# Optimization experiments

Hardware: AMD Instinct MI355X
Metric: run time of the kernel (lower is better)

Reference implementation:

```python
import jax, jax.numpy as jnp
import numpy as np
import math

B, T = 4, 2048
V = 512          # vocab_size
D = 256          # d_model
H = 4            # n_heads
NLAYERS = 2
DH = D // H      # d_head = 64
NB = DH // 2     # n_blocks = 32
R = 2            # bottleneck_r
DFF = 4 * D
GRID = 64
EPS = 1e-5


def setup_inputs() -> dict:
    key = jax.random.key(0)
    ks = iter(jax.random.split(key, 32))
    def nrm(shape, s=0.02):
        return jax.random.normal(next(ks), shape, dtype=jnp.float32) * s
    tokens = jax.random.randint(next(ks), (B, T), 0, V)
    token_emb = nrm((V, D))
    # low-rank action-to-Lie projection
    w_in = nrm((D, R))
    w_out = nrm((R, H * NB))
    # geometric omega init (PathIntegrator.__init__)
    frac = jnp.arange(NB, dtype=jnp.float32) / max(NB - 1, 1)
    omega = jnp.broadcast_to(2.0 * math.pi * (1.0 / GRID) ** frac, (H, NB)).astype(jnp.float32)
    # stacked per-layer params (weights stored [in, out])
    Wq = nrm((NLAYERS, D, D)); bq = jnp.zeros((NLAYERS, D), jnp.float32)
    Wk = nrm((NLAYERS, D, D)); bk = jnp.zeros((NLAYERS, D), jnp.float32)
    Wv = nrm((NLAYERS, D, D)); bv = jnp.zeros((NLAYERS, D), jnp.float32)
    Wo = nrm((NLAYERS, D, D)); bo = jnp.zeros((NLAYERS, D), jnp.float32)
    ln1_g = jnp.ones((NLAYERS, D), jnp.float32); ln1_b = jnp.zeros((NLAYERS, D), jnp.float32)
    ln2_g = jnp.ones((NLAYERS, D), jnp.float32); ln2_b = jnp.zeros((NLAYERS, D), jnp.float32)
    W1 = nrm((NLAYERS, D, DFF)); b1 = jnp.zeros((NLAYERS, DFF), jnp.float32)
    W2 = nrm((NLAYERS, DFF, D)); b2 = jnp.zeros((NLAYERS, D), jnp.float32)
    out_g = jnp.ones((D,), jnp.float32); out_b = jnp.zeros((D,), jnp.float32)
    Wout = nrm((D, V)); bout = jnp.zeros((V,), jnp.float32)
    return dict(tokens=tokens, token_emb=token_emb, w_in=w_in, w_out=w_out, omega=omega,
                Wq=Wq, bq=bq, Wk=Wk, bk=bk, Wv=Wv, bv=bv, Wo=Wo, bo=bo,
                ln1_g=ln1_g, ln1_b=ln1_b, ln2_g=ln2_g, ln2_b=ln2_b,
                W1=W1, b1=b1, W2=W2, b2=b2, out_g=out_g, out_b=out_b,
                Wout=Wout, bout=bout)


def _ln(x, g, b):
    mu = jnp.mean(x, axis=-1, keepdims=True)
    xc = x - mu
    var = jnp.mean(xc * xc, axis=-1, keepdims=True)
    return xc * jax.lax.rsqrt(var + EPS) * g + b


def _rope(x, cos, sin):
    # x: (B,H,T,DH); cos/sin: (B,H,T,NB) with NB = DH//2 (interleaved pairs)
    x1 = x[..., 0::2]
    x2 = x[..., 1::2]
    o1 = x1 * cos - x2 * sin
    o2 = x1 * sin + x2 * cos
    return jnp.stack([o1, o2], axis=-1).reshape(x.shape)


def reference(tokens, token_emb, w_in, w_out, omega, Wq, bq, Wk, bk, Wv, bv, Wo, bo,
              ln1_g, ln1_b, ln2_g, ln2_b, W1, b1, W2, b2, out_g, out_b, Wout, bout):
    Bx, Tx = tokens.shape
    x = token_emb[tokens]                                   # (B,T,D)
    # action -> Lie algebra deltas (low rank)
    delta = ((x @ w_in) @ w_out).reshape(Bx, Tx, H, NB)     # (B,T,H,NB)
    # path integrator: cumulative angles
    angles = jnp.cumsum(delta, axis=1) * omega[None, None]  # (B,T,H,NB)
    angles = angles.transpose(0, 2, 1, 3)                   # (B,H,T,NB)
    cos_a, sin_a = jnp.cos(angles), jnp.sin(angles)
    causal = jnp.triu(jnp.ones((Tx, Tx), bool), 1)          # True = masked
    neg = jnp.finfo(x.dtype).min
    scale = 1.0 / math.sqrt(DH)
    for i in range(NLAYERS):
        h = _ln(x, ln1_g[i], ln1_b[i])
        Q = (h @ Wq[i] + bq[i]).reshape(Bx, Tx, H, DH).transpose(0, 2, 1, 3)
        K = (h @ Wk[i] + bk[i]).reshape(Bx, Tx, H, DH).transpose(0, 2, 1, 3)
        Vv = (h @ Wv[i] + bv[i]).reshape(Bx, Tx, H, DH).transpose(0, 2, 1, 3)
        Q = _rope(Q, cos_a, sin_a)
        K = _rope(K, cos_a, sin_a)
        scores = jnp.einsum('bhqd,bhkd->bhqk', Q, K) * scale
        scores = jnp.where(causal, neg, scores)
        attn = jax.nn.softmax(scores, axis=-1)
        out = jnp.einsum('bhqk,bhkd->bhqd', attn, Vv)
        out = out.transpose(0, 2, 1, 3).reshape(Bx, Tx, D)
        x = x + out @ Wo[i] + bo[i]
        h2 = _ln(x, ln2_g[i], ln2_b[i])
        x = x + jax.nn.gelu(h2 @ W1[i] + b1[i], approximate=False) @ W2[i] + b2[i]
    x = _ln(x, out_g, out_b)
    return x @ Wout + bout                                   # (B,T,V)
```

## Files before the change

### kernel.cpp

```cpp
#include <hip/hip_runtime.h>
#include <hip/hip_bf16.h>
#include <math.h>

#define B_   4
#define T_   2048
#define V_   512
#define D_   256
#define H_   4
#define DH_  64
#define NB_  32
#define DFF_ 1024
#define NL_  2

typedef __attribute__((ext_vector_type(8))) short short8_t;
typedef __attribute__((ext_vector_type(4))) float float4_t;

#define MFMA16(a,b,c) __builtin_amdgcn_mfma_f32_16x16x32_bf16(a,b,c,0,0,0)

__device__ __forceinline__ unsigned short f2bf_bits(float f) {
    unsigned u = __float_as_uint(f);
    u += 0x7fffu + ((u >> 16) & 1u);
    return (unsigned short)(u >> 16);
}

__global__ __launch_bounds__(256) void wt_kernel(
    const float* __restrict__ Wq, const float* __restrict__ Wk,
    const float* __restrict__ Wv, const float* __restrict__ Wo,
    const float* __restrict__ W1, const float* __restrict__ W2,
    const float* __restrict__ Wout,
    unsigned short* __restrict__ wqt, unsigned short* __restrict__ wkt,
    unsigned short* __restrict__ wvt, unsigned short* __restrict__ wot,
    unsigned short* __restrict__ w1t, unsigned short* __restrict__ w2t,
    unsigned short* __restrict__ woutt)
{
    __shared__ float tile[32][33];
    int bx = blockIdx.x, tid = threadIdx.x;
    const float* src; unsigned short* dst; int Kd, Nd, tr, tc;
    if (bx < 512) {
        int am = bx >> 6, t = bx & 63;
        const float* s4[4] = {Wq, Wk, Wv, Wo};
        unsigned short* d4[4] = {wqt, wkt, wvt, wot};
        src = s4[am >> 1] + (long)(am & 1) * 65536;
        dst = d4[am >> 1] + (long)(am & 1) * 65536;
        Kd = 256; Nd = 256; tr = t >> 3; tc = t & 7;
    } else if (bx < 1024) {
        int idx = bx - 512, mat = idx >> 8, t = idx & 255;
        src = W1 + (long)mat * 262144; dst = w1t + (long)mat * 262144;
        Kd = 256; Nd = 1024; tr = t >> 5; tc = t & 31;
    } else if (bx < 1536) {
        int idx = bx - 1024, mat = idx >> 8, t = idx & 255;
        src = W2 + (long)mat * 262144; dst = w2t + (long)mat * 262144;
        Kd = 1024; Nd = 256; tr = t >> 3; tc = t & 7;
    } else {
        int t = bx - 1536;
        src = Wout; dst = woutt; Kd = 256; Nd = 512; tr = t >> 4; tc = t & 15;
    }
    int kr = tid >> 3, nc4 = (tid & 7) * 4;
    float4_t v = *(const float4_t*)&src[(long)(tr * 32 + kr) * Nd + tc * 32 + nc4];
    for (int j = 0; j < 4; ++j) tile[kr][nc4 + j] = v[j];
    __syncthreads();
    int nr = tid >> 3, kc4 = (tid & 7) * 4;
    unsigned short tmp[4];
    for (int j = 0; j < 4; ++j) tmp[j] = f2bf_bits(tile[kc4 + j][nr]);
    uint2 uu;
    uu.x = (unsigned)tmp[0] | ((unsigned)tmp[1] << 16);
    uu.y = (unsigned)tmp[2] | ((unsigned)tmp[3] << 16);
    *(uint2*)&dst[(long)(tc * 32 + nr) * Kd + tr * 32 + kc4] = uu;
}

__global__ __launch_bounds__(256) void embed_kernel(
    const int* __restrict__ tokens, const float* __restrict__ emb,
    const float* __restrict__ w_in, const float* __restrict__ w_out,
    float* __restrict__ x, float* __restrict__ delta)
{
    int bt = blockIdx.x;
    int d  = threadIdx.x;
    int tok = tokens[bt];
    float e = emb[tok * D_ + d];
    x[(long)bt * D_ + d] = e;

    __shared__ float r0s[256], r1s[256];
    r0s[d] = e * w_in[d * 2 + 0];
    r1s[d] = e * w_in[d * 2 + 1];
    __syncthreads();
    for (int off = 128; off > 0; off >>= 1) {
        if (d < off) { r0s[d] += r0s[d + off]; r1s[d] += r1s[d + off]; }
        __syncthreads();
    }
    float r0 = r0s[0], r1 = r1s[0];
    if (d < H_ * NB_) {
        delta[(long)bt * (H_ * NB_) + d] =
            r0 * w_out[d] + r1 * w_out[H_ * NB_ + d];
    }
}

__global__ __launch_bounds__(256) void cumsum_kernel(
    const float* __restrict__ delta, const float* __restrict__ omega,
    float* __restrict__ cosb, float* __restrict__ sinb)
{
    int c = blockIdx.x & (H_ * NB_ - 1);
    int b = blockIdx.x >> 7;
    int tid = threadIdx.x;
    float om = omega[c];
    int h = c >> 5, nb = c & (NB_ - 1);

    float vals[8];
    float s = 0.0f;
    for (int i = 0; i < 8; ++i) {
        int t = tid * 8 + i;
        vals[i] = delta[((long)b * T_ + t) * (H_ * NB_) + c];
        s += vals[i];
    }
    __shared__ float sc[256];
    sc[tid] = s;
    __syncthreads();
    for (int off = 1; off < 256; off <<= 1) {
        float v = (tid >= off) ? sc[tid - off] : 0.0f;
        __syncthreads();
        sc[tid] += v;
        __syncthreads();
    }
    float run = sc[tid] - s;
    for (int i = 0; i < 8; ++i) {
        run += vals[i];
        float ang = run * om;
        int t = tid * 8 + i;
        long oi = ((long)(b * H_ + h) * T_ + t) * NB_ + nb;
        cosb[oi] = cosf(ang);
        sinb[oi] = sinf(ang);
    }
}

__global__ __launch_bounds__(256) void ln_kernel(
    const float* __restrict__ x, const float* __restrict__ g,
    const float* __restrict__ b, unsigned short* __restrict__ out)
{
    int w = threadIdx.x >> 6, lane = threadIdx.x & 63;
    long row = (long)blockIdx.x * 4 + w;
    float4_t v = *(const float4_t*)&x[row * D_ + lane * 4];
    float s = v[0] + v[1] + v[2] + v[3];
    float q = v[0]*v[0] + v[1]*v[1] + v[2]*v[2] + v[3]*v[3];
    for (int off = 1; off < 64; off <<= 1) {
        s += __shfl_xor(s, off);
        q += __shfl_xor(q, off);
    }
    float mu  = s * (1.0f / D_);
    float var = q * (1.0f / D_) - mu * mu;
    float inv = rsqrtf(var + 1e-5f);
    float4_t gg = *(const float4_t*)&g[lane * 4];
    float4_t bb = *(const float4_t*)&b[lane * 4];
    unsigned short h0 = f2bf_bits((v[0] - mu) * inv * gg[0] + bb[0]);
    unsigned short h1 = f2bf_bits((v[1] - mu) * inv * gg[1] + bb[1]);
    unsigned short h2 = f2bf_bits((v[2] - mu) * inv * gg[2] + bb[2]);
    unsigned short h3 = f2bf_bits((v[3] - mu) * inv * gg[3] + bb[3]);
    uint2 uu;
    uu.x = (unsigned)h0 | ((unsigned)h1 << 16);
    uu.y = (unsigned)h2 | ((unsigned)h3 << 16);
    *(uint2*)&out[row * D_ + lane * 4] = uu;
}

__global__ __launch_bounds__(256) void gemm_mfma(
    const unsigned short* __restrict__ A, const unsigned short* __restrict__ Bt,
    const float* __restrict__ bias, const float* __restrict__ res,
    float* __restrict__ outf, unsigned short* __restrict__ outb,
    const float* __restrict__ ropeC, const float* __restrict__ ropeS,
    float qscale, int M, int N, int K, int mode, int do_gelu)
{
    __shared__ __align__(16) short As[64 * 72];
    __shared__ __align__(16) short Bs[64 * 72];
    int tid = threadIdx.x;
    int w = tid >> 6, lane = tid & 63, quad = lane >> 4, l16 = lane & 15;
    int n0 = blockIdx.x * 64, r0 = blockIdx.y * 64;

    float4_t acc[4];
    for (int nt = 0; nt < 4; ++nt) acc[nt] = (float4_t){0.f, 0.f, 0.f, 0.f};

    for (int k0 = 0; k0 < K; k0 += 64) {
        __syncthreads();
        for (int i = 0; i < 2; ++i) {
            int e = tid + 256 * i;
            int r = e >> 3, c8 = e & 7;
            *(short8_t*)&As[r * 72 + c8 * 8] =
                *(const short8_t*)&A[(long)(r0 + r) * K + k0 + c8 * 8];
            *(short8_t*)&Bs[r * 72 + c8 * 8] =
                *(const short8_t*)&Bt[(long)(n0 + r) * K + k0 + c8 * 8];
        }
        __syncthreads();
        for (int kq = 0; kq < 2; ++kq) {
            short8_t a = *(const short8_t*)&As[(w * 16 + l16) * 72 + kq * 32 + quad * 8];
            for (int nt = 0; nt < 4; ++nt) {
                short8_t bfr = *(const short8_t*)&Bs[(nt * 16 + l16) * 72 + kq * 32 + quad * 8];
                acc[nt] = MFMA16(a, bfr, acc[nt]);
            }
        }
    }

    int h_head = n0 >> 6;
    for (int nt = 0; nt < 4; ++nt) {
        int n = n0 + nt * 16 + l16;
        float bcol = (mode == 2) ? 0.0f : bias[n];
        for (int r = 0; r < 4; ++r) {
            int row = r0 + w * 16 + quad * 4 + r;
            float v = acc[nt][r] + ((mode == 2) ? bias[row] : bcol);
            if (res) v += res[(long)row * N + n];
            if (do_gelu) v = 0.5f * v * (1.0f + erff(v * 0.70710678118654752f));
            if (mode == 0) {
                outf[(long)row * N + n] = v;
            } else if (mode == 1 || mode == 2) {
                outb[(long)row * N + n] = f2bf_bits(v);
            } else {
                float vp = __shfl_xor(v, 1);
                int bb = row >> 11, t = row & (T_ - 1);
                int nb = (n & 63) >> 1;
                long ci = ((long)(bb * H_ + h_head) * T_ + t) * NB_ + nb;
                float c = ropeC[ci], sn = ropeS[ci];
                float ov = (l16 & 1) ? (vp * sn + v * c) : (v * c - vp * sn);
                outb[((long)(bb * H_ + h_head) * T_ + t) * DH_ + (n & 63)] =
                    f2bf_bits(ov * qscale);
            }
        }
    }
}

__global__ __launch_bounds__(512) void attn_mfma(
    const unsigned short* __restrict__ Qb, const unsigned short* __restrict__ Kb,
    const unsigned short* __restrict__ Vt, unsigned short* __restrict__ O)
{
    __shared__ __align__(16) short KsS[2][64 * 72];
    __shared__ __align__(16) short VsS[2][64 * 72];
    union PsOm { short Ps[8][16 * 72]; float Om[4][16 * 66]; };
    __shared__ __align__(16) PsOm U;
    __shared__ float Ml[4][16][2];

    int tid = threadIdx.x;
    int w = tid >> 6, lane = tid & 63;
    int quad = lane >> 4, l16 = lane & 15;
    int bh = blockIdx.x & 15;
    int p  = blockIdx.x >> 4;
    int wr = w & 3;
    int g  = w >> 2;
    int b = bh >> 2, h = bh & 3;
    int qtS = 31 - p;

    const unsigned short* kgb = Kb + (long)bh * T_ * DH_;
    const unsigned short* vgb = Vt + (long)h * DH_ * (B_ * T_) + (long)b * T_;
    short* PsW = &U.Ps[w][0];

    int row0 = wr * 16 + (lane >> 3);
    int c80  = (lane & 7) * 8;

    int q0 = (g == 0 ? p : qtS) * 64;
    int qglob = q0 + wr * 16 + l16;
    const unsigned short* qp =
        Qb + ((long)bh * T_ + q0 + wr * 16 + l16) * DH_ + quad * 8;
    short8_t aq[2];
    aq[0] = *(const short8_t*)qp;
    aq[1] = *(const short8_t*)(qp + 32);

    float m_r = -3.0e38f, l_r = 0.0f;
    float4_t o[4];
    for (int nt = 0; nt < 4; ++nt) o[nt] = (float4_t){0.f, 0.f, 0.f, 0.f};

    {
        int k0n = (g == 0) ? 0 : (16 - p) * 64;
        for (int i = 0; i < 2; ++i) {
            int row = row0 + 8 * i;
            short8_t kv = *(const short8_t*)&kgb[(long)(k0n + row) * DH_ + c80];
            short8_t vv = *(const short8_t*)&vgb[(long)row * (B_ * T_) + k0n + c80];
            *(short8_t*)&KsS[g][row * 72 + c80] = kv;
            *(short8_t*)&VsS[g][row * 72 + c80] = vv;
        }
    }
    __syncthreads();

    for (int j = 0; j < 17; ++j) {
        bool idle  = (g == 1) && (j == 16);
        bool haveN = (j < 16) && !((g == 1) && (j == 15));

        short8_t stK[2], stV[2];
        if (haveN) {
            int jn = j + 1;
            int k0n = (g == 0) ? ((jn <= p) ? jn * 64 : (jn - p - 1) * 64)
                               : (16 - p + jn) * 64;
            for (int i = 0; i < 2; ++i) {
                int row = row0 + 8 * i;
                stK[i] = *(const short8_t*)&kgb[(long)(k0n + row) * DH_ + c80];
                stV[i] = *(const short8_t*)&vgb[(long)row * (B_ * T_) + k0n + c80];
            }
        }

        if (!idle) {
            int k0 = (g == 0) ? ((j <= p) ? j * 64 : (j - p - 1) * 64)
                              : (16 - p + j) * 64;
            bool msk = (g == 0) ? (j == p) : (j == 15);

            short8_t kf[4][2], vb[4][2];
            for (int nt = 0; nt < 4; ++nt) {
                const short* kb_ = &KsS[g][(nt * 16 + l16) * 72 + quad * 8];
                const short* vb_ = &VsS[g][(nt * 16 + l16) * 72 + quad * 8];
                kf[nt][0] = *(const short8_t*)kb_;
                kf[nt][1] = *(const short8_t*)(kb_ + 32);
                vb[nt][0] = *(const short8_t*)vb_;
                vb[nt][1] = *(const short8_t*)(vb_ + 32);
            }

            float4_t st[4];
            for (int nt = 0; nt < 4; ++nt) {
                float4_t sa = (float4_t){0.f, 0.f, 0.f, 0.f};
                sa = MFMA16(kf[nt][0], aq[0], sa);
                sa = MFMA16(kf[nt][1], aq[1], sa);
                st[nt] = sa;
            }

            float mt = -3.0e38f;
            for (int nt = 0; nt < 4; ++nt) {
                for (int r = 0; r < 4; ++r) {
                    float sv = st[nt][r];
                    if (msk && (k0 + nt * 16 + quad * 4 + r) > qglob) sv = -3.0e38f;
                    st[nt][r] = sv;
                    mt = fmaxf(mt, sv);
                }
            }
            mt = fmaxf(mt, __shfl_xor(mt, 16));
            mt = fmaxf(mt, __shfl_xor(mt, 32));

            float mn = fmaxf(m_r, mt);
            float alpha = __expf(m_r - mn);
            m_r = mn;

            float ac[4];
            for (int r = 0; r < 4; ++r) ac[r] = __shfl(alpha, quad * 4 + r);

            float lt = 0.0f;
            for (int nt = 0; nt < 4; ++nt) {
                for (int r = 0; r < 4; ++r) {
                    float pv = __expf(st[nt][r] - m_r);
                    lt += pv;
                    PsW[l16 * 72 + nt * 16 + quad * 4 + r] = (short)f2bf_bits(pv);
                }
            }
            lt += __shfl_xor(lt, 16);
            lt += __shfl_xor(lt, 32);
            l_r = l_r * alpha + lt;

            for (int nt = 0; nt < 4; ++nt)
                for (int r = 0; r < 4; ++r) o[nt][r] *= ac[r];

            for (int kq = 0; kq < 2; ++kq) {
                short8_t pa = *(const short8_t*)&PsW[l16 * 72 + kq * 32 + quad * 8];
                for (int nt = 0; nt < 4; ++nt)
                    o[nt] = MFMA16(pa, vb[nt][kq], o[nt]);
            }

            if (g == 0 && j == p) {
                float linv[4];
                for (int r = 0; r < 4; ++r) linv[r] = __shfl(l_r, quad * 4 + r);
                for (int r = 0; r < 4; ++r) {
                    float inv = 1.0f / linv[r];
                    int trow = p * 64 + wr * 16 + quad * 4 + r;
                    long orow = ((long)b * T_ + trow) * D_ + h * 64;
                    for (int nt = 0; nt < 4; ++nt)
                        O[orow + nt * 16 + l16] = f2bf_bits(o[nt][r] * inv);
                }
                m_r = -3.0e38f; l_r = 0.0f;
                for (int nt = 0; nt < 4; ++nt) o[nt] = (float4_t){0.f, 0.f, 0.f, 0.f};
                const unsigned short* qp2 =
                    Qb + ((long)bh * T_ + qtS * 64 + wr * 16 + l16) * DH_ + quad * 8;
                aq[0] = *(const short8_t*)qp2;
                aq[1] = *(const short8_t*)(qp2 + 32);
                qglob = qtS * 64 + wr * 16 + l16;
            }
        }

        if (j < 16) {
            __syncthreads();
            if (haveN) {
                for (int i = 0; i < 2; ++i) {
                    int row = row0 + 8 * i;
                    *(short8_t*)&KsS[g][row * 72 + c80] = stK[i];
                    *(short8_t*)&VsS[g][row * 72 + c80] = stV[i];
                }
            }
            __syncthreads();
        }
    }

    __syncthreads();
    if (g == 0) {
        for (int nt = 0; nt < 4; ++nt)
            for (int r = 0; r < 4; ++r)
                U.Om[wr][(quad * 4 + r) * 66 + nt * 16 + l16] = o[nt][r];
        if (quad == 0) { Ml[wr][l16][0] = m_r; Ml[wr][l16][1] = l_r; }
    }
    __syncthreads();
    if (g == 1) {
        int q0s = qtS * 64;
        for (int r = 0; r < 4; ++r) {
            int row = quad * 4 + r;
            float mA = Ml[wr][row][0], lA = Ml[wr][row][1];
            float mB = __shfl(m_r, row);
            float lB = __shfl(l_r, row);
            float M  = fmaxf(mA, mB);
            float eA = __expf(mA - M), eB = __expf(mB - M);
            float inv = 1.0f / (lA * eA + lB * eB);
            int trow = q0s + wr * 16 + row;
            long orow = ((long)b * T_ + trow) * D_ + h * 64;
            for (int nt = 0; nt < 4; ++nt) {
                float vm = U.Om[wr][row * 66 + nt * 16 + l16] * eA + o[nt][r] * eB;
                O[orow + nt * 16 + l16] = f2bf_bits(vm * inv);
            }
        }
    }
}

extern "C" void kernel_launch(void* const* d_in, const int* in_sizes, int n_in,
                              void* d_out, int out_size, void* d_ws, size_t ws_size,
                              hipStream_t stream)
{
    const int*   tokens    = (const int*)d_in[0];
    const float* token_emb = (const float*)d_in[1];
    const float* w_in      = (const float*)d_in[2];
    const float* w_out     = (const float*)d_in[3];
    const float* omega     = (const float*)d_in[4];
    const float* Wq        = (const float*)d_in[5];
    const float* bq        = (const float*)d_in[6];
    const float* Wk        = (const float*)d_in[7];
    const float* bk        = (const float*)d_in[8];
    const float* Wv        = (const float*)d_in[9];
    const float* bv        = (const float*)d_in[10];
    const float* Wo        = (const float*)d_in[11];
    const float* bo        = (const float*)d_in[12];
    const float* ln1_g     = (const float*)d_in[13];
    const float* ln1_b     = (const float*)d_in[14];
    const float* ln2_g     = (const float*)d_in[15];
    const float* ln2_b     = (const float*)d_in[16];
    const float* W1        = (const float*)d_in[17];
    const float* b1        = (const float*)d_in[18];
    const float* W2        = (const float*)d_in[19];
    const float* b2        = (const float*)d_in[20];
    const float* out_g     = (const float*)d_in[21];
    const float* out_b     = (const float*)d_in[22];
    const float* Wout      = (const float*)d_in[23];
    const float* bout      = (const float*)d_in[24];

    const long NTOK = (long)B_ * T_;
    float* xbuf = (float*)d_ws;
    float* cosb = xbuf + NTOK * D_;
    float* sinb = cosb + NTOK * H_ * NB_;
    float* dbuf = sinb + NTOK * H_ * NB_;
    unsigned short* hbuf  = (unsigned short*)(dbuf + NTOK * H_ * NB_);
    unsigned short* obuf  = hbuf + NTOK * D_;
    unsigned short* ffbuf = obuf + NTOK * D_;
    unsigned short* qb16  = ffbuf + NTOK * DFF_;
    unsigned short* kb16  = qb16 + NTOK * D_;
    unsigned short* vtb   = kb16 + NTOK * D_;
    unsigned short* wqt   = vtb + NTOK * D_;
    unsigned short* wkt   = wqt + 2 * 65536;
    unsigned short* wvt   = wkt + 2 * 65536;
    unsigned short* wot   = wvt + 2 * 65536;
    unsigned short* w1t   = wot + 2 * 65536;
    unsigned short* w2t   = w1t + 2 * 262144;
    unsigned short* woutt = w2t + 2 * 262144;

    wt_kernel<<<1664, 256, 0, stream>>>(Wq, Wk, Wv, Wo, W1, W2, Wout,
                                        wqt, wkt, wvt, wot, w1t, w2t, woutt);
    embed_kernel<<<NTOK, 256, 0, stream>>>(tokens, token_emb, w_in, w_out, xbuf, dbuf);
    cumsum_kernel<<<B_ * H_ * NB_, 256, 0, stream>>>(dbuf, omega, cosb, sinb);

    for (int l = 0; l < NL_; ++l) {
        ln_kernel<<<2048, 256, 0, stream>>>(xbuf, ln1_g + l * D_, ln1_b + l * D_, hbuf);
        gemm_mfma<<<dim3(4, 128), 256, 0, stream>>>(
            hbuf, wqt + (long)l * 65536, bq + l * D_, nullptr, nullptr, qb16,
            cosb, sinb, 0.125f, (int)NTOK, D_, D_, 3, 0);
        gemm_mfma<<<dim3(4, 128), 256, 0, stream>>>(
            hbuf, wkt + (long)l * 65536, bk + l * D_, nullptr, nullptr, kb16,
            cosb, sinb, 1.0f, (int)NTOK, D_, D_, 3, 0);
        gemm_mfma<<<dim3(128, 4), 256, 0, stream>>>(
            wvt + (long)l * 65536, hbuf, bv + l * D_, nullptr, nullptr, vtb,
            nullptr, nullptr, 0.f, D_, (int)NTOK, D_, 2, 0);
        attn_mfma<<<256, 512, 0, stream>>>(qb16, kb16, vtb, obuf);
        gemm_mfma<<<dim3(4, 128), 256, 0, stream>>>(
            obuf, wot + (long)l * 65536, bo + l * D_, xbuf, xbuf, nullptr,
            nullptr, nullptr, 0.f, (int)NTOK, D_, D_, 0, 0);
        ln_kernel<<<2048, 256, 0, stream>>>(xbuf, ln2_g + l * D_, ln2_b + l * D_, hbuf);
        gemm_mfma<<<dim3(16, 128), 256, 0, stream>>>(
            hbuf, w1t + (long)l * 262144, b1 + l * DFF_, nullptr, nullptr, ffbuf,
            nullptr, nullptr, 0.f, (int)NTOK, DFF_, D_, 1, 1);
        gemm_mfma<<<dim3(4, 128), 256, 0, stream>>>(
            ffbuf, w2t + (long)l * 262144, b2 + l * D_, xbuf, xbuf, nullptr,
            nullptr, nullptr, 0.f, (int)NTOK, D_, DFF_, 0, 0);
    }

    ln_kernel<<<2048, 256, 0, stream>>>(xbuf, out_g, out_b, hbuf);
    gemm_mfma<<<dim3(8, 128), 256, 0, stream>>>(
        hbuf, woutt, bout, nullptr, (float*)d_out, nullptr,
        nullptr, nullptr, 0.f, (int)NTOK, V_, D_, 0, 0);
}
```

Measured before the change: 438.2 us.

## Enlarge GEMM tiles, prefetch K-slices in registers, fuse Q and K projections

Measured after the change: 585.5 us. 1.34x slower.

```diff
diff --git a/kernel.cpp b/kernel.cpp
--- a/kernel.cpp
+++ b/kernel.cpp
@@ -28,7 +28,7 @@
     const float* __restrict__ Wv, const float* __restrict__ Wo,
     const float* __restrict__ W1, const float* __restrict__ W2,
     const float* __restrict__ Wout,
-    unsigned short* __restrict__ wqt, unsigned short* __restrict__ wkt,
+    unsigned short* __restrict__ wqkt,
     unsigned short* __restrict__ wvt, unsigned short* __restrict__ wot,
     unsigned short* __restrict__ w1t, unsigned short* __restrict__ w2t,
     unsigned short* __restrict__ woutt)
@@ -38,10 +38,13 @@
     const float* src; unsigned short* dst; int Kd, Nd, tr, tc;
     if (bx < 512) {
         int am = bx >> 6, t = bx & 63;
+        int m4 = am >> 1, layer = am & 1;
         const float* s4[4] = {Wq, Wk, Wv, Wo};
-        unsigned short* d4[4] = {wqt, wkt, wvt, wot};
-        src = s4[am >> 1] + (long)(am & 1) * 65536;
-        dst = d4[am >> 1] + (long)(am & 1) * 65536;
+        src = s4[m4] + (long)layer * 65536;
+        if (m4 == 0)      dst = wqkt + (long)layer * 131072;
+        else if (m4 == 1) dst = wqkt + (long)layer * 131072 + 65536;
+        else if (m4 == 2) dst = wvt + (long)layer * 65536;
+        else              dst = wot + (long)layer * 65536;
         Kd = 256; Nd = 256; tr = t >> 3; tc = t & 7;
     } else if (bx < 1024) {
         int idx = bx - 512, mat = idx >> 8, t = idx & 255;
@@ -159,64 +162,111 @@
     *(uint2*)&out[row * D_ + lane * 4] = uu;
 }
 
+template<int BN>
 __global__ __launch_bounds__(256) void gemm_mfma(
     const unsigned short* __restrict__ A, const unsigned short* __restrict__ Bt,
-    const float* __restrict__ bias, const float* __restrict__ res,
+    const float* __restrict__ bias, const float* __restrict__ bias2,
+    const float* __restrict__ res,
     float* __restrict__ outf, unsigned short* __restrict__ outb,
     const float* __restrict__ ropeC, const float* __restrict__ ropeS,
-    float qscale, int M, int N, int K, int mode, int do_gelu)
-{
-    __shared__ __align__(16) short As[64 * 72];
-    __shared__ __align__(16) short Bs[64 * 72];
+    int M, int N, int K, int mode, int do_gelu)
+{
+    constexpr int NT  = BN / 16;
+    constexpr int BCH = BN / 32;
+    __shared__ __align__(16) short As[128 * 72];
+    __shared__ __align__(16) short Bs[BN * 72];
+
     int tid = threadIdx.x;
     int w = tid >> 6, lane = tid & 63, quad = lane >> 4, l16 = lane & 15;
-    int n0 = blockIdx.x * 64, r0 = blockIdx.y * 64;
-
-    float4_t acc[4];
-    for (int nt = 0; nt < 4; ++nt) acc[nt] = (float4_t){0.f, 0.f, 0.f, 0.f};
-
-    for (int k0 = 0; k0 < K; k0 += 64) {
+    int n0 = blockIdx.x * BN, r0 = blockIdx.y * 128;
+
+    float4_t acc[2][NT];
+    for (int m = 0; m < 2; ++m)
+        for (int nt = 0; nt < NT; ++nt) acc[m][nt] = (float4_t){0.f, 0.f, 0.f, 0.f};
+
+    short8_t sA[4], sB[BCH];
+    for (int i = 0; i < 4; ++i) {
+        int e = tid + 256 * i, row = e >> 3, c8 = e & 7;
+        sA[i] = *(const short8_t*)&A[(long)(r0 + row) * K + c8 * 8];
+    }
+    for (int i = 0; i < BCH; ++i) {
+        int e = tid + 256 * i, row = e >> 3, c8 = e & 7;
+        sB[i] = *(const short8_t*)&Bt[(long)(n0 + row) * K + c8 * 8];
+    }
+    for (int i = 0; i < 4; ++i) {
+        int e = tid + 256 * i, row = e >> 3, c8 = e & 7;
+        *(short8_t*)&As[row * 72 + c8 * 8] = sA[i];
+    }
+    for (int i = 0; i < BCH; ++i) {
+        int e = tid + 256 * i, row = e >> 3, c8 = e & 7;
+        *(short8_t*)&Bs[row * 72 + c8 * 8] = sB[i];
+    }
+    __syncthreads();
+
+    for (int k0 = 0;; k0 += 64) {
+        bool have = (k0 + 64 < K);
+        if (have) {
+            for (int i = 0; i < 4; ++i) {
+                int e = tid + 256 * i, row = e >> 3, c8 = e & 7;
+                sA[i] = *(const short8_t*)&A[(long)(r0 + row) * K + k0 + 64 + c8 * 8];
+            }
+            for (int i = 0; i < BCH; ++i) {
+                int e = tid + 256 * i, row = e >> 3, c8 = e & 7;
+                sB[i] = *(const short8_t*)&Bt[(long)(n0 + row) * K + k0 + 64 + c8 * 8];
+            }
+        }
+        for (int kq = 0; kq < 2; ++kq) {
+            short8_t bf[NT];
+            for (int nt = 0; nt < NT; ++nt)
+                bf[nt] = *(const short8_t*)&Bs[(nt * 16 + l16) * 72 + kq * 32 + quad * 8];
+            for (int m = 0; m < 2; ++m) {
+                short8_t a = *(const short8_t*)&As[(w * 32 + m * 16 + l16) * 72 + kq * 32 + quad * 8];
+                for (int nt = 0; nt < NT; ++nt)
+                    acc[m][nt] = MFMA16(a, bf[nt], acc[m][nt]);
+            }
+        }
+        if (!have) break;
         __syncthreads();
-        for (int i = 0; i < 2; ++i) {
-            int e = tid + 256 * i;
-            int r = e >> 3, c8 = e & 7;
-            *(short8_t*)&As[r * 72 + c8 * 8] =
-                *(const short8_t*)&A[(long)(r0 + r) * K + k0 + c8 * 8];
-            *(short8_t*)&Bs[r * 72 + c8 * 8] =
-                *(const short8_t*)&Bt[(long)(n0 + r) * K + k0 + c8 * 8];
+        for (int i = 0; i < 4; ++i) {
+            int e = tid + 256 * i, row = e >> 3, c8 = e & 7;
+            *(short8_t*)&As[row * 72 + c8 * 8] = sA[i];
+        }
+        for (int i = 0; i < BCH; ++i) {
+            int e = tid + 256 * i, row = e >> 3, c8 = e & 7;
+            *(short8_t*)&Bs[row * 72 + c8 * 8] = sB[i];
         }
         __syncthreads();
-        for (int kq = 0; kq < 2; ++kq) {
-            short8_t a = *(const short8_t*)&As[(w * 16 + l16) * 72 + kq * 32 + quad * 8];
-            for (int nt = 0; nt < 4; ++nt) {
-                short8_t bfr = *(const short8_t*)&Bs[(nt * 16 + l16) * 72 + kq * 32 + quad * 8];
-                acc[nt] = MFMA16(a, bfr, acc[nt]);
-            }
-        }
-    }
-
-    int h_head = n0 >> 6;
-    for (int nt = 0; nt < 4; ++nt) {
-        int n = n0 + nt * 16 + l16;
-        float bcol = (mode == 2) ? 0.0f : bias[n];
-        for (int r = 0; r < 4; ++r) {
-            int row = r0 + w * 16 + quad * 4 + r;
-            float v = acc[nt][r] + ((mode == 2) ? bias[row] : bcol);
-            if (res) v += res[(long)row * N + n];
-            if (do_gelu) v = 0.5f * v * (1.0f + erff(v * 0.70710678118654752f));
-            if (mode == 0) {
-                outf[(long)row * N + n] = v;
-            } else if (mode == 1 || mode == 2) {
-                outb[(long)row * N + n] = f2bf_bits(v);
-            } else {
-                float vp = __shfl_xor(v, 1);
-                int bb = row >> 11, t = row & (T_ - 1);
-                int nb = (n & 63) >> 1;
-                long ci = ((long)(bb * H_ + h_head) * T_ + t) * NB_ + nb;
-                float c = ropeC[ci], sn = ropeS[ci];
-                float ov = (l16 & 1) ? (vp * sn + v * c) : (v * c - vp * sn);
-                outb[((long)(bb * H_ + h_head) * T_ + t) * DH_ + (n & 63)] =
-                    f2bf_bits(ov * qscale);
+    }
+
+    for (int m = 0; m < 2; ++m) {
+        for (int nt = 0; nt < NT; ++nt) {
+            int n = n0 + nt * 16 + l16;
+            for (int r = 0; r < 4; ++r) {
+                int row = r0 + w * 32 + m * 16 + quad * 4 + r;
+                float v = acc[m][nt][r];
+                if (mode == 2)      v += bias[row];
+                else if (mode == 3) v += (n < 256) ? bias[n] : bias2[n - 256];
+                else                v += bias[n];
+                if (res) v += res[(long)row * N + n];
+                if (do_gelu) v = 0.5f * v * (1.0f + erff(v * 0.70710678118654752f));
+                if (mode == 0) {
+                    outf[(long)row * N + n] = v;
+                } else if (mode <= 2) {
+                    outb[(long)row * N + n] = f2bf_bits(v);
+                } else {
+                    float vp = __shfl_xor(v, 1);
+                    bool isK = (n >= 256);
+                    int nn = isK ? n - 256 : n;
+                    int bb = row >> 11, t = row & (T_ - 1);
+                    int hh = nn >> 6, nb = (nn & 63) >> 1;
+                    long ci = ((long)(bb * H_ + hh) * T_ + t) * NB_ + nb;
+                    float c = ropeC[ci], sn = ropeS[ci];
+                    float ov = (l16 & 1) ? (vp * sn + v * c) : (v * c - vp * sn);
+                    float qs = isK ? 1.0f : 0.125f;
+                    long off = isK ? (long)B_ * T_ * D_ : 0;
+                    outb[off + ((long)(bb * H_ + hh) * T_ + t) * DH_ + (nn & 63)] =
+                        f2bf_bits(ov * qs);
+                }
             }
         }
     }
@@ -454,45 +504,41 @@
     unsigned short* qb16  = ffbuf + NTOK * DFF_;
     unsigned short* kb16  = qb16 + NTOK * D_;
     unsigned short* vtb   = kb16 + NTOK * D_;
-    unsigned short* wqt   = vtb + NTOK * D_;
-    unsigned short* wkt   = wqt + 2 * 65536;
-    unsigned short* wvt   = wkt + 2 * 65536;
+    unsigned short* wqkt  = vtb + NTOK * D_;
+    unsigned short* wvt   = wqkt + 2 * 131072;
     unsigned short* wot   = wvt + 2 * 65536;
     unsigned short* w1t   = wot + 2 * 65536;
     unsigned short* w2t   = w1t + 2 * 262144;
     unsigned short* woutt = w2t + 2 * 262144;
 
     wt_kernel<<<1664, 256, 0, stream>>>(Wq, Wk, Wv, Wo, W1, W2, Wout,
-                                        wqt, wkt, wvt, wot, w1t, w2t, woutt);
+                                        wqkt, wvt, wot, w1t, w2t, woutt);
     embed_kernel<<<NTOK, 256, 0, stream>>>(tokens, token_emb, w_in, w_out, xbuf, dbuf);
     cumsum_kernel<<<B_ * H_ * NB_, 256, 0, stream>>>(dbuf, omega, cosb, sinb);
 
     for (int l = 0; l < NL_; ++l) {
         ln_kernel<<<2048, 256, 0, stream>>>(xbuf, ln1_g + l * D_, ln1_b + l * D_, hbuf);
-        gemm_mfma<<<dim3(4, 128), 256, 0, stream>>>(
-            hbuf, wqt + (long)l * 65536, bq + l * D_, nullptr, nullptr, qb16,
-            cosb, sinb, 0.125f, (int)NTOK, D_, D_, 3, 0);
-        gemm_mfma<<<dim3(4, 128), 256, 0, stream>>>(
-            hbuf, wkt + (long)l * 65536, bk + l * D_, nullptr, nullptr, kb16,
-            cosb, sinb, 1.0f, (int)NTOK, D_, D_, 3, 0);
-        gemm_mfma<<<dim3(128, 4), 256, 0, stream>>>(
-            wvt + (long)l * 65536, hbuf, bv + l * D_, nullptr, nullptr, vtb,
-            nullptr, nullptr, 0.f, D_, (int)NTOK, D_, 2, 0);
+        gemm_mfma<64><<<dim3(8, 64), 256, 0, stream>>>(
+            hbuf, wqkt + (long)l * 131072, bq + l * D_, bk + l * D_, nullptr,
+            nullptr, qb16, cosb, sinb, (int)NTOK, 512, 256, 3, 0);
+        gemm_mfma<64><<<dim3(128, 2), 256, 0, stream>>>(
+            wvt + (long)l * 65536, hbuf, bv + l * D_, nullptr, nullptr,
+            nullptr, vtb, nullptr, nullptr, 256, (int)NTOK, 256, 2, 0);
         attn_mfma<<<256, 512, 0, stream>>>(qb16, kb16, vtb, obuf);
-        gemm_mfma<<<dim3(4, 128), 256, 0, stream>>>(
-            obuf, wot + (long)l * 65536, bo + l * D_, xbuf, xbuf, nullptr,
-            nullptr, nullptr, 0.f, (int)NTOK, D_, D_, 0, 0);
+        gemm_mfma<64><<<dim3(4, 64), 256, 0, stream>>>(
+            obuf, wot + (long)l * 65536, bo + l * D_, nullptr, xbuf,
+            xbuf, nullptr, nullptr, nullptr, (int)NTOK, 256, 256, 0, 0);
         ln_kernel<<<2048, 256, 0, stream>>>(xbuf, ln2_g + l * D_, ln2_b + l * D_, hbuf);
-        gemm_mfma<<<dim3(16, 128), 256, 0, stream>>>(
-            hbuf, w1t + (long)l * 262144, b1 + l * DFF_, nullptr, nullptr, ffbuf,
-            nullptr, nullptr, 0.f, (int)NTOK, DFF_, D_, 1, 1);
-        gemm_mfma<<<dim3(4, 128), 256, 0, stream>>>(
-            ffbuf, w2t + (long)l * 262144, b2 + l * D_, xbuf, xbuf, nullptr,
-            nullptr, nullptr, 0.f, (int)NTOK, D_, DFF_, 0, 0);
+        gemm_mfma<128><<<dim3(8, 64), 256, 0, stream>>>(
+            hbuf, w1t + (long)l * 262144, b1 + l * DFF_, nullptr, nullptr,
+            nullptr, ffbuf, nullptr, nullptr, (int)NTOK, DFF_, 256, 1, 1);
+        gemm_mfma<64><<<dim3(4, 64), 256, 0, stream>>>(
+            ffbuf, w2t + (long)l * 262144, b2 + l * D_, nullptr, xbuf,
+            xbuf, nullptr, nullptr, nullptr, (int)NTOK, 256, 1024, 0, 0);
     }
 
     ln_kernel<<<2048, 256, 0, stream>>>(xbuf, out_g, out_b, hbuf);
-    gemm_mfma<<<dim3(8, 128), 256, 0, stream>>>(
-        hbuf, woutt, bout, nullptr, (float*)d_out, nullptr,
-        nullptr, nullptr, 0.f, (int)NTOK, V_, D_, 0, 0);
-}
+    gemm_mfma<64><<<dim3(8, 64), 256, 0, stream>>>(
+        hbuf, woutt, bout, nullptr, nullptr,
+        (float*)d_out, nullptr, nullptr, nullptr, (int)NTOK, V_, 256, 0, 0);
+}
```
